# Kernel tuning notes

Hardware: AMD Instinct MI355X
Metric: run time of the kernel (lower is better)

## Reference

```python
import jax, jax.numpy as jnp
import numpy as np

TEMP = 0.5
EPS = 1e-8  # torch CosineSimilarity eps
B, D = 8192, 128


def _normalize(x):
    # torch cosine_similarity: x / max(||x||, eps)
    n = jnp.linalg.norm(x, axis=-1, keepdims=True)
    return x / jnp.maximum(n, EPS)


def setup_inputs() -> dict:
    key = jax.random.key(0)
    k1, k2 = jax.random.split(key)
    zis = jax.random.normal(k1, (B, D), dtype=jnp.float32)
    zjs = jax.random.normal(k2, (B, D), dtype=jnp.float32)
    partnet_ids = jnp.arange(B, dtype=jnp.int32)  # unique ids
    return {"zis": zis, "zjs": zjs, "partnet_ids": partnet_ids}


def reference(zis, zjs, partnet_ids):
    b = zis.shape[0]
    zi_n = _normalize(zis)
    zj_n = _normalize(zjs)
    # full pairwise cosine similarities (one GEMM each), scaled by temperature
    s_ij = jnp.einsum('id,jd->ij', zi_n, zj_n) / TEMP  # zis vs zjs, [B,B]
    s_ik = jnp.einsum('id,kd->ik', zi_n, zi_n) / TEMP  # zis vs zis, [B,B]
    # negatives: off-diagonal AND different partnet id
    eye = jnp.eye(b, dtype=bool)
    same_id = partnet_ids[:, None] == partnet_ids[None, :]
    neg_mask = (~eye) & (~same_id)
    neg_inf = jnp.float32(-jnp.inf)
    # positive: with unique ids the original loop keeps the j==i pair -> diagonal
    pos = jnp.diagonal(s_ij)  # [B]
    logits = jnp.concatenate([
        pos[:, None],
        jnp.where(neg_mask, s_ij, neg_inf),
        jnp.where(neg_mask, s_ik, neg_inf),
    ], axis=1)  # [B, 1+2B]
    # CrossEntropyLoss(label=0, reduction='sum') per row = logsumexp - pos
    lse = jax.nn.logsumexp(logits, axis=1)
    final_loss = jnp.sum(lse - pos)
    return final_loss / (2.0 * b)
```

## Files before the change

kernel.cpp:

```cpp
#include <hip/hip_runtime.h>
#include <stdint.h>

#define BDIM 8192
#define DDIM 128
#define NCHUNK 16
#define ROWS_PER_BLOCK 256
#define COLS_PER_BLOCK (2 * BDIM / NCHUNK)
#define TCOLS 32
#define NT (COLS_PER_BLOCK / TCOLS)

#if __has_builtin(__builtin_amdgcn_global_load_lds)
#define HAS_GLOAD_LDS 1
#else
#define HAS_GLOAD_LDS 0
#endif

constexpr float TEMP_ = 0.5f;
constexpr float LOG2E = 1.4426950408889634f;
constexpr float LN2F = 0.6931471805599453f;
constexpr float QSCALE = LOG2E / TEMP_;

typedef __attribute__((ext_vector_type(8))) short bf16x8;
typedef __attribute__((ext_vector_type(4))) float f32x4;

__device__ inline float fexp2(float x) {
#if __has_builtin(__builtin_amdgcn_exp2f)
  return __builtin_amdgcn_exp2f(x);
#else
  return exp2f(x);
#endif
}

__device__ inline float flog2(float x) {
#if __has_builtin(__builtin_amdgcn_logf)
  return __builtin_amdgcn_logf(x);
#else
  return log2f(x);
#endif
}

#if HAS_GLOAD_LDS
__device__ inline void gload_lds16(const void* g, void* l) {
  __builtin_amdgcn_global_load_lds(
      (const __attribute__((address_space(1))) void*)g,
      (__attribute__((address_space(3))) void*)l, 16, 0, 0);
}
#endif

__device__ inline unsigned short f2bf(float f) {
  unsigned int u = __float_as_uint(f);
  u += 0x7FFFu + ((u >> 16) & 1u);
  return (unsigned short)(u >> 16);
}

__global__ __launch_bounds__(256) void nk(const float* __restrict__ zis,
                                          const float* __restrict__ zjs,
                                          unsigned short* __restrict__ qs,
                                          unsigned short* __restrict__ kc,
                                          float* __restrict__ post) {
  const int wid = threadIdx.x >> 6;
  const int lane = threadIdx.x & 63;
  const int row = blockIdx.x * 4 + wid;
  const float2 zi = *(const float2*)(zis + (size_t)row * DDIM + lane * 2);
  const float2 zj = *(const float2*)(zjs + (size_t)row * DDIM + lane * 2);
  float ssi = zi.x * zi.x + zi.y * zi.y;
  float ssj = zj.x * zj.x + zj.y * zj.y;
  float dot = zi.x * zj.x + zi.y * zj.y;
#pragma unroll
  for (int off = 32; off >= 1; off >>= 1) {
    ssi += __shfl_xor(ssi, off);
    ssj += __shfl_xor(ssj, off);
    dot += __shfl_xor(dot, off);
  }
  const float invi = 1.0f / fmaxf(sqrtf(ssi), 1e-8f);
  const float invj = 1.0f / fmaxf(sqrtf(ssj), 1e-8f);
  const float tpos = dot * invi * invj * (1.0f / TEMP_);

  const float qi0 = zi.x * invi, qi1 = zi.y * invi;
  const float qj0 = zj.x * invj, qj1 = zj.y * invj;

  ushort2 w;
  w.x = f2bf(qi0 * QSCALE); w.y = f2bf(qi1 * QSCALE);
  *(ushort2*)(qs + (size_t)row * DDIM + lane * 2) = w;
  w.x = f2bf(qj0); w.y = f2bf(qj1);
  *(ushort2*)(kc + (size_t)row * DDIM + lane * 2) = w;
  w.x = f2bf(qi0); w.y = f2bf(qi1);
  *(ushort2*)(kc + (size_t)(BDIM + row) * DDIM + lane * 2) = w;

  if (lane == 0) post[row] = tpos;
}

__global__ __launch_bounds__(512, 4) void mk(const unsigned short* __restrict__ qs,
                                             const unsigned short* __restrict__ kc,
                                             const int* __restrict__ ids,
                                             float* __restrict__ su) {
  __shared__ char lds[2 * 8192 + COLS_PER_BLOCK * 4];
  int* ids_l = (int*)(lds + 16384);

  const int tid = threadIdx.x;
  const int wid = tid >> 6;
  const int lane = tid & 63;
  const int qr = lane & 15;
  const int kg = lane >> 4;

  const int swz = (blockIdx.x & 7) * 64 + (blockIdx.x >> 3);
  const int rb = swz & 31;
  const int cb = swz >> 5;
  const int q0 = rb * ROWS_PER_BLOCK + wid * 32;
  const int c0 = cb * COLS_PER_BLOCK;

#pragma unroll
  for (int c = tid; c < COLS_PER_BLOCK; c += 512)
    ids_l[c] = ids[(c0 + c) & (BDIM - 1)];

  bf16x8 qA[4], qB[4];
  const unsigned short* qbaseA = qs + (size_t)(q0 + qr) * DDIM + kg * 8;
  const unsigned short* qbaseB = qbaseA + 16 * DDIM;
#pragma unroll
  for (int kk = 0; kk < 4; kk++) {
    qA[kk] = *(const bf16x8*)(qbaseA + kk * 32);
    qB[kk] = *(const bf16x8*)(qbaseB + kk * 32);
  }
  const int idA = ids[q0 + qr];
  const int idB = ids[q0 + 16 + qr];

  const int scol = tid >> 4;
  const int sslot = tid & 15;
  const char* kcb = (const char*)kc;
  const int gsoff = scol * 256 + ((sslot * 16) ^ ((scol & 7) << 4));
#if HAS_GLOAD_LDS
  char* ldst = lds + wid * 1024;
#endif

  int cur = 0;
#if HAS_GLOAD_LDS
  gload_lds16(kcb + (size_t)(c0) * 256 + gsoff, ldst);
#else
  *(int4*)(lds + tid * 16) = *(const int4*)(kcb + (size_t)(c0) * 256 + gsoff);
#endif
  __syncthreads();

  f32x4 acc[2][2] = {{{0.f, 0.f, 0.f, 0.f}, {0.f, 0.f, 0.f, 0.f}},
                     {{0.f, 0.f, 0.f, 0.f}, {0.f, 0.f, 0.f, 0.f}}};

  for (int t = 0; t < NT; ++t) {
#if !HAS_GLOAD_LDS
    int4 pf;
#endif
    if (t + 1 < NT) {
      const char* gp = kcb + (size_t)(c0 + (t + 1) * TCOLS) * 256 + gsoff;
#if HAS_GLOAD_LDS
      gload_lds16(gp, ldst + (cur ^ 1) * 8192);
#else
      pf = *(const int4*)gp;
#endif
    }

    const char* kb = lds + cur * 8192;
#pragma unroll
    for (int cg = 0; cg < 2; ++cg) {
      const int col = cg * 16 + qr;
      const char* abase = kb + col * 256;
      f32x4 aT0 = {0.f, 0.f, 0.f, 0.f};
      f32x4 aT1 = {0.f, 0.f, 0.f, 0.f};
#pragma unroll
      for (int kk = 0; kk < 4; ++kk) {
        const int off = (kk * 64 + kg * 16) ^ ((qr & 7) << 4);
        const bf16x8 af = *(const bf16x8*)(abase + off);
        aT0 = __builtin_amdgcn_mfma_f32_16x16x32_bf16(af, qA[kk], aT0, 0, 0, 0);
        aT1 = __builtin_amdgcn_mfma_f32_16x16x32_bf16(af, qB[kk], aT1, 0, 0, 0);
      }
      const int4 idv = *(const int4*)&ids_l[t * TCOLS + cg * 16 + kg * 4];
#pragma unroll
      for (int r = 0; r < 4; ++r) {
        const int idc = (&idv.x)[r];
        acc[cg][0][r] += (idc == idA) ? 0.0f : fexp2(aT0[r]);
        acc[cg][1][r] += (idc == idB) ? 0.0f : fexp2(aT1[r]);
      }
    }
#if !HAS_GLOAD_LDS
    if (t + 1 < NT) *(int4*)(lds + (cur ^ 1) * 8192 + tid * 16) = pf;
#endif
    __syncthreads();
    cur ^= 1;
  }

  float sA = acc[0][0][0] + acc[0][0][1] + acc[0][0][2] + acc[0][0][3] +
             acc[1][0][0] + acc[1][0][1] + acc[1][0][2] + acc[1][0][3];
  float sB = acc[0][1][0] + acc[0][1][1] + acc[0][1][2] + acc[0][1][3] +
             acc[1][1][0] + acc[1][1][1] + acc[1][1][2] + acc[1][1][3];
  sA += __shfl_xor(sA, 16); sA += __shfl_xor(sA, 32);
  sB += __shfl_xor(sB, 16); sB += __shfl_xor(sB, 32);
  if (lane < 16) {
    atomicAdd(&su[q0 + lane], sA);
    atomicAdd(&su[q0 + 16 + lane], sB);
  }
}

__global__ __launch_bounds__(256) void fk(const float* __restrict__ su,
                                          const float* __restrict__ post,
                                          float* __restrict__ out) {
  const int i = blockIdx.x * 256 + threadIdx.x;
  const float tp = post[i];
  const float v = su[i] + fexp2(tp * LOG2E);
  float c = (LN2F * flog2(v) - tp) * (1.0f / (2.0f * BDIM));
#pragma unroll
  for (int off = 32; off >= 1; off >>= 1) c += __shfl_xor(c, off);
  if ((threadIdx.x & 63) == 0) atomicAdd(out, c);
}

extern "C" void kernel_launch(void* const* d_in, const int* in_sizes, int n_in,
                              void* d_out, int out_size, void* d_ws, size_t ws_size,
                              hipStream_t stream) {
  const float* zis = (const float*)d_in[0];
  const float* zjs = (const float*)d_in[1];
  const int* ids = (const int*)d_in[2];

  char* ws = (char*)d_ws;
  unsigned short* qs = (unsigned short*)ws;
  unsigned short* kc = (unsigned short*)(ws + (size_t)2 * 1024 * 1024);
  float* post = (float*)(ws + (size_t)6 * 1024 * 1024);
  float* su = (float*)(ws + (size_t)6 * 1024 * 1024 + 32768);

  hipMemsetAsync(d_out, 0, sizeof(float), stream);
  hipMemsetAsync(su, 0, BDIM * sizeof(float), stream);

  nk<<<BDIM / 4, 256, 0, stream>>>(zis, zjs, qs, kc, post);
  mk<<<32 * NCHUNK, 512, 0, stream>>>(qs, kc, ids, su);
  fk<<<BDIM / 256, 256, 0, stream>>>(su, post, (float*)d_out);
}
```

Measured before the change: 115.8 us.

## Give each wave its own double-buffered K stream, removing block barriers

Result: slower. 156.0 us (+34.7%).

```diff
diff --git a/kernel.cpp b/kernel.cpp
--- a/kernel.cpp
+++ b/kernel.cpp
@@ -3,11 +3,10 @@
 
 #define BDIM 8192
 #define DDIM 128
-#define NCHUNK 16
-#define ROWS_PER_BLOCK 256
-#define COLS_PER_BLOCK (2 * BDIM / NCHUNK)
-#define TCOLS 32
-#define NT (COLS_PER_BLOCK / TCOLS)
+#define WC 256
+#define TCOLS 16
+#define NS (WC / TCOLS)
+#define NBLK 4096
 
 #if __has_builtin(__builtin_amdgcn_global_load_lds)
 #define HAS_GLOAD_LDS 1
@@ -90,12 +89,11 @@
   if (lane == 0) post[row] = tpos;
 }
 
-__global__ __launch_bounds__(512, 4) void mk(const unsigned short* __restrict__ qs,
+__global__ __launch_bounds__(256, 5) void mk(const unsigned short* __restrict__ qs,
                                              const unsigned short* __restrict__ kc,
                                              const int* __restrict__ ids,
                                              float* __restrict__ su) {
-  __shared__ char lds[2 * 8192 + COLS_PER_BLOCK * 4];
-  int* ids_l = (int*)(lds + 16384);
+  __shared__ char lds[4 * 8192];
 
   const int tid = threadIdx.x;
   const int wid = tid >> 6;
@@ -103,15 +101,12 @@
   const int qr = lane & 15;
   const int kg = lane >> 4;
 
-  const int swz = (blockIdx.x & 7) * 64 + (blockIdx.x >> 3);
-  const int rb = swz & 31;
-  const int cb = swz >> 5;
-  const int q0 = rb * ROWS_PER_BLOCK + wid * 32;
-  const int c0 = cb * COLS_PER_BLOCK;
-
-#pragma unroll
-  for (int c = tid; c < COLS_PER_BLOCK; c += 512)
-    ids_l[c] = ids[(c0 + c) & (BDIM - 1)];
+  const int b = blockIdx.x;
+  const int j = (b >> 3) * 4 + wid;
+  const int cp = (b & 7) * 8 + (j & 7);
+  const int rs = j >> 3;
+  const int q0 = rs * 32;
+  const int c0 = cp * WC;
 
   bf16x8 qA[4], qB[4];
   const unsigned short* qbaseA = qs + (size_t)(q0 + qr) * DDIM + kg * 8;
@@ -124,71 +119,79 @@
   const int idA = ids[q0 + qr];
   const int idB = ids[q0 + 16 + qr];
 
-  const int scol = tid >> 4;
-  const int sslot = tid & 15;
+  char* wavebuf = lds + wid * 8192;
   const char* kcb = (const char*)kc;
-  const int gsoff = scol * 256 + ((sslot * 16) ^ ((scol & 7) << 4));
+  int gsoff[4];
+#pragma unroll
+  for (int g = 0; g < 4; ++g) {
+    const int scol = g * 4 + (lane >> 4);
+    gsoff[g] = scol * 256 + (((lane & 15) * 16) ^ ((scol & 15) << 4));
+  }
+  int roff[4];
+#pragma unroll
+  for (int kk = 0; kk < 4; ++kk)
+    roff[kk] = qr * 256 + ((kk * 64 + kg * 16) ^ ((qr & 15) << 4));
+
+  {
+    const char* kstep = kcb + (size_t)c0 * 256;
+#pragma unroll
+    for (int g = 0; g < 4; ++g) {
 #if HAS_GLOAD_LDS
-  char* ldst = lds + wid * 1024;
-#endif
-
-  int cur = 0;
+      gload_lds16(kstep + gsoff[g], wavebuf + g * 1024);
+#else
+      *(int4*)(wavebuf + g * 1024 + lane * 16) = *(const int4*)(kstep + gsoff[g]);
+#endif
+    }
+  }
+
+  f32x4 acc0 = {0.f, 0.f, 0.f, 0.f};
+  f32x4 acc1 = {0.f, 0.f, 0.f, 0.f};
+
+#pragma unroll 2
+  for (int st = 0; st < NS; ++st) {
+    const int cur = st & 1;
+    const char* kb = wavebuf + cur * 4096;
+
+    asm volatile("s_waitcnt vmcnt(0)" ::: "memory");
+
+    bf16x8 af[4];
+#pragma unroll
+    for (int kk = 0; kk < 4; ++kk)
+      af[kk] = *(const bf16x8*)(kb + roff[kk]);
+
+    const int4 idv =
+        *(const int4*)(ids + ((c0 + st * TCOLS + kg * 4) & (BDIM - 1)));
+
+    if (st + 1 < NS) {
+      const char* kstep = kcb + (size_t)(c0 + (st + 1) * TCOLS) * 256;
+      char* dst = wavebuf + (cur ^ 1) * 4096;
+#pragma unroll
+      for (int g = 0; g < 4; ++g) {
 #if HAS_GLOAD_LDS
-  gload_lds16(kcb + (size_t)(c0) * 256 + gsoff, ldst);
-#else
-  *(int4*)(lds + tid * 16) = *(const int4*)(kcb + (size_t)(c0) * 256 + gsoff);
-#endif
-  __syncthreads();
-
-  f32x4 acc[2][2] = {{{0.f, 0.f, 0.f, 0.f}, {0.f, 0.f, 0.f, 0.f}},
-                     {{0.f, 0.f, 0.f, 0.f}, {0.f, 0.f, 0.f, 0.f}}};
-
-  for (int t = 0; t < NT; ++t) {
-#if !HAS_GLOAD_LDS
-    int4 pf;
-#endif
-    if (t + 1 < NT) {
-      const char* gp = kcb + (size_t)(c0 + (t + 1) * TCOLS) * 256 + gsoff;
-#if HAS_GLOAD_LDS
-      gload_lds16(gp, ldst + (cur ^ 1) * 8192);
-#else
-      pf = *(const int4*)gp;
-#endif
-    }
-
-    const char* kb = lds + cur * 8192;
-#pragma unroll
-    for (int cg = 0; cg < 2; ++cg) {
-      const int col = cg * 16 + qr;
-      const char* abase = kb + col * 256;
-      f32x4 aT0 = {0.f, 0.f, 0.f, 0.f};
-      f32x4 aT1 = {0.f, 0.f, 0.f, 0.f};
-#pragma unroll
-      for (int kk = 0; kk < 4; ++kk) {
-        const int off = (kk * 64 + kg * 16) ^ ((qr & 7) << 4);
-        const bf16x8 af = *(const bf16x8*)(abase + off);
-        aT0 = __builtin_amdgcn_mfma_f32_16x16x32_bf16(af, qA[kk], aT0, 0, 0, 0);
-        aT1 = __builtin_amdgcn_mfma_f32_16x16x32_bf16(af, qB[kk], aT1, 0, 0, 0);
+        gload_lds16(kstep + gsoff[g], dst + g * 1024);
+#else
+        *(int4*)(dst + g * 1024 + lane * 16) = *(const int4*)(kstep + gsoff[g]);
+#endif
       }
-      const int4 idv = *(const int4*)&ids_l[t * TCOLS + cg * 16 + kg * 4];
-#pragma unroll
-      for (int r = 0; r < 4; ++r) {
-        const int idc = (&idv.x)[r];
-        acc[cg][0][r] += (idc == idA) ? 0.0f : fexp2(aT0[r]);
-        acc[cg][1][r] += (idc == idB) ? 0.0f : fexp2(aT1[r]);
-      }
-    }
-#if !HAS_GLOAD_LDS
-    if (t + 1 < NT) *(int4*)(lds + (cur ^ 1) * 8192 + tid * 16) = pf;
-#endif
-    __syncthreads();
-    cur ^= 1;
-  }
-
-  float sA = acc[0][0][0] + acc[0][0][1] + acc[0][0][2] + acc[0][0][3] +
-             acc[1][0][0] + acc[1][0][1] + acc[1][0][2] + acc[1][0][3];
-  float sB = acc[0][1][0] + acc[0][1][1] + acc[0][1][2] + acc[0][1][3] +
-             acc[1][1][0] + acc[1][1][1] + acc[1][1][2] + acc[1][1][3];
+    }
+
+    f32x4 aT0 = {0.f, 0.f, 0.f, 0.f};
+    f32x4 aT1 = {0.f, 0.f, 0.f, 0.f};
+#pragma unroll
+    for (int kk = 0; kk < 4; ++kk) {
+      aT0 = __builtin_amdgcn_mfma_f32_16x16x32_bf16(af[kk], qA[kk], aT0, 0, 0, 0);
+      aT1 = __builtin_amdgcn_mfma_f32_16x16x32_bf16(af[kk], qB[kk], aT1, 0, 0, 0);
+    }
+#pragma unroll
+    for (int r = 0; r < 4; ++r) {
+      const int idc = (&idv.x)[r];
+      acc0[r] += (idc == idA) ? 0.0f : fexp2(aT0[r]);
+      acc1[r] += (idc == idB) ? 0.0f : fexp2(aT1[r]);
+    }
+  }
+
+  float sA = acc0[0] + acc0[1] + acc0[2] + acc0[3];
+  float sB = acc1[0] + acc1[1] + acc1[2] + acc1[3];
   sA += __shfl_xor(sA, 16); sA += __shfl_xor(sA, 32);
   sB += __shfl_xor(sB, 16); sB += __shfl_xor(sB, 32);
   if (lane < 16) {
@@ -226,6 +229,6 @@
   hipMemsetAsync(su, 0, BDIM * sizeof(float), stream);
 
   nk<<<BDIM / 4, 256, 0, stream>>>(zis, zjs, qs, kc, post);
-  mk<<<32 * NCHUNK, 512, 0, stream>>>(qs, kc, ids, su);
+  mk<<<NBLK, 256, 0, stream>>>(qs, kc, ids, su);
   fk<<<BDIM / 256, 256, 0, stream>>>(su, post, (float*)d_out);
 }
```
